# Kernel tuning notes

Measured on AMD Instinct MI355X. Metric: run time of the kernel, lower is better.

Reference implementation:

```python
import jax, jax.numpy as jnp
import numpy as np

KEHALF = 7.199822675975274  # half Coulomb constant, eV*Angstrom/e^2
SR_CUTOFF = 4.0
LR_CUTOFF = 10.0
N_ATOMS = 262144
N_PAIRS = 16777216


def setup_inputs() -> dict:
    key = jax.random.key(0)
    k1, k2, k3, k4 = jax.random.split(key, 4)
    # distances in (0.1, 12.1) Angstrom: spans both cutoffs, avoids r=0 singularity
    Dij = jax.random.uniform(k1, (N_PAIRS,), dtype=jnp.float32) * 12.0 + 0.1
    Qa = jax.random.normal(k2, (N_ATOMS,), dtype=jnp.float32) * 0.3  # partial charges
    idx_i = jax.random.randint(k3, (N_PAIRS,), 0, N_ATOMS, dtype=jnp.int64)
    idx_j = jax.random.randint(k4, (N_PAIRS,), 0, N_ATOMS, dtype=jnp.int64)
    return {"Dij": Dij, "Qa": Qa, "idx_i": idx_i, "idx_j": idx_j}


def _poly_cutoff(r, cutoff):
    x = r / cutoff
    return jnp.where(x < 1.0, 1.0 - x * x * x * (x * (6.0 * x - 15.0) + 10.0), 0.0)


def reference(Dij, Qa, idx_i, idx_j):
    lr2 = LR_CUTOFF * LR_CUTOFF
    Qi = Qa[idx_i]                      # [P]
    Qj = Qa[idx_j]                      # [P]
    Dij_sh = jnp.sqrt(Dij * Dij + 1.0)  # shielded distance
    switch = _poly_cutoff(Dij, SR_CUTOFF / 2.0)  # phi(2r) with cutoff sr
    cswitch = 1.0 - switch
    E_ord = 1.0 / Dij + Dij / lr2 - 2.0 / LR_CUTOFF
    E_sh = 1.0 / Dij_sh + Dij_sh / lr2 - 2.0 / LR_CUTOFF
    Eele = KEHALF * Qi * Qj * (switch * E_sh + cswitch * E_ord)
    Eele = jnp.where(Dij <= LR_CUTOFF, Eele, 0.0)
    # scatter-add per-pair energies to atoms
    return jax.ops.segment_sum(Eele, idx_i, num_segments=Qa.shape[0])
```

## Files before the change

kernel.cpp:

```cpp
#include <hip/hip_runtime.h>


#define KEHALF 7.199822675975274f
#define NB    128
#define BSH   11
#define BMASK 2047
#define CAP   126976
#define CURSTRIDE 16
#define SCH   2
#define SCAP  72
#define SSTR  73
#define VSCALE 524288.0f
#define VINV   (1.0f / 524288.0f)
#define P1B   512
#define P1PAIRS 8192

__device__ __forceinline__ float radial_fast(float d) {
    float d2p1 = d * d + 1.0f;
    float rsq  = __builtin_amdgcn_rsqf(d2p1);
    float x    = 0.5f * d;
    float sw   = (x < 1.0f) ? 1.0f - x * x * x * (x * (6.0f * x - 15.0f) + 10.0f)
                            : 0.0f;
    float Eo = __builtin_amdgcn_rcpf(d) + d * 0.01f - 0.2f;
    float Es = rsq * (1.0f + 0.01f * d2p1) - 0.2f;
    return sw * Es + (1.0f - sw) * Eo;
}

__global__ __launch_bounds__(P1B, 4) void ee_bin(
    const float* __restrict__ Dij,
    const float* __restrict__ Qa,
    const int*   __restrict__ idx_i,
    const int*   __restrict__ idx_j,
    unsigned int* __restrict__ list,
    unsigned int* __restrict__ gcur,
    float*        __restrict__ out)
{
    __shared__ unsigned int stage[NB * SSTR];
    __shared__ int lcur[NB + 32];
    __shared__ int gofs[NB];
    int tid = threadIdx.x;
    if (tid < NB + 32) lcur[tid] = 0;
    __syncthreads();

    long blockBase = (long)blockIdx.x * P1PAIRS;

    unsigned int EN[16];
    int          BK[16];
    int trash = NB + (tid & 31);
#pragma unroll
    for (int g = 0; g < 4; ++g) {
        long o = blockBase + ((long)(g * P1B + tid)) * 4;
        int4 j4 = *reinterpret_cast<const int4*>(idx_j + o);
        float qj0 = Qa[j4.x], qj1 = Qa[j4.y], qj2 = Qa[j4.z], qj3 = Qa[j4.w];
        float4 d4 = *reinterpret_cast<const float4*>(Dij + o);
        int4   i4 = *reinterpret_cast<const int4*>(idx_i + o);
        float dd[4] = {d4.x, d4.y, d4.z, d4.w};
        float qq[4] = {qj0, qj1, qj2, qj3};
        int   ii[4] = {i4.x, i4.y, i4.z, i4.w};
#pragma unroll
        for (int k = 0; k < 4; ++k) {
            int m = g * 4 + k;
            float d = dd[k];
            float w = qq[k] * radial_fast(d);
            int v = __float2int_rn(w * VSCALE);
            EN[m] = ((unsigned int)(ii[k] & BMASK) << 21) |
                    ((unsigned int)v & 0x1FFFFFu);
            BK[m] = (d <= 10.0f) ? (ii[k] >> BSH) : trash;
        }
    }

    int SL[16];
#pragma unroll
    for (int m = 0; m < 16; ++m)
        SL[m] = atomicAdd(&lcur[BK[m]], 1);

#pragma unroll
    for (int m = 0; m < 16; ++m) {
        if (BK[m] < NB) {
            if (SL[m] < SCAP) {
                stage[BK[m] * SSTR + SL[m]] = EN[m];
            } else {
                int atom = (BK[m] << BSH) | (int)(EN[m] >> 21);
                int v    = ((int)(EN[m] << 11)) >> 11;
                atomicAdd(out + atom, KEHALF * Qa[atom] * ((float)v * VINV));
            }
        }
    }
    __syncthreads();

    if (tid < NB) {
        int n = lcur[tid];
        if (n > SCAP) n = SCAP;
        lcur[tid] = n;
        int padded = (n + 3) & ~3;
        gofs[tid] = (int)atomicAdd(&gcur[tid * CURSTRIDE], (unsigned int)padded);
    }
    __syncthreads();

    int wave = tid >> 6, lane = tid & 63;
    for (int b = wave; b < NB; b += (P1B / 64)) {
        int n = lcur[b];
        int padded = (n + 3) & ~3;
        int go = gofs[b];
        long rb = (long)b * CAP;
        for (int i = lane; i < padded; i += 64) {
            unsigned int val = (i < n) ? stage[b * SSTR + i]
                                       : ((unsigned int)(i & BMASK) << 21);
            int pos = go + i;
            if (pos < CAP)
                list[rb + pos] = val;
        }
    }
}

__global__ __launch_bounds__(512) void ee_acc(
    const unsigned int* __restrict__ list,
    const unsigned int* __restrict__ gcur,
    int* __restrict__ partials)
{
    __shared__ int acc[1 << BSH];
    int b = blockIdx.x / SCH;
    int s = blockIdx.x % SCH;
    int t = threadIdx.x;
#pragma unroll
    for (int r = 0; r < (1 << BSH) / 512; ++r) acc[t + r * 512] = 0;
    __syncthreads();

    int n = (int)gcur[b * CURSTRIDE];
    if (n > CAP) n = CAP;
    int nq = n >> 2;
    int per = (nq + SCH - 1) / SCH;
    int q0 = s * per;
    int q1 = q0 + per; if (q1 > nq) q1 = nq;

    const uint4* lp4 = reinterpret_cast<const uint4*>(list + (long)b * CAP);
    for (int q = q0 + t; q < q1; q += 512) {
        uint4 u4 = lp4[q];
        unsigned int us[4] = {u4.x, u4.y, u4.z, u4.w};
#pragma unroll
        for (int k = 0; k < 4; ++k) {
            unsigned int u = us[k];
            int li = (int)(u >> 21);
            int v  = ((int)(u << 11)) >> 11;
            atomicAdd(&acc[li], v);
        }
    }
    __syncthreads();

    int* pp = partials + ((long)b * SCH + s) * (1 << BSH);
#pragma unroll
    for (int r = 0; r < (1 << BSH) / 512; ++r) pp[t + r * 512] = acc[t + r * 512];
}

__global__ __launch_bounds__(256) void ee_final(
    const int* __restrict__ partials,
    const float* __restrict__ Qa,
    float* __restrict__ out, int nAtoms)
{
    int q = blockIdx.x * blockDim.x + threadIdx.x;
    int n4 = nAtoms >> 2;
    if (q >= n4) return;
    int a0 = q << 2;
    int b  = a0 >> BSH;
    int li = a0 & BMASK;
    long base = (long)(b * SCH) * (1 << BSH) + li;
    int4 s = {0, 0, 0, 0};
#pragma unroll
    for (int r = 0; r < SCH; ++r) {
        int4 p = *reinterpret_cast<const int4*>(partials + base + (long)r * (1 << BSH));
        s.x += p.x; s.y += p.y; s.z += p.z; s.w += p.w;
    }
    float4 qv = reinterpret_cast<const float4*>(Qa)[q];
    float4 sp = reinterpret_cast<const float4*>(out)[q];
    float4 o;
    o.x = KEHALF * qv.x * ((float)s.x * VINV) + sp.x;
    o.y = KEHALF * qv.y * ((float)s.y * VINV) + sp.y;
    o.z = KEHALF * qv.z * ((float)s.z * VINV) + sp.z;
    o.w = KEHALF * qv.w * ((float)s.w * VINV) + sp.w;
    reinterpret_cast<float4*>(out)[q] = o;
}

#define FP_SCALE 4194304.0f
#define FP_INV   (1.0f / 4194304.0f)

__device__ __forceinline__ float radial_exact(float d) {
    float dsh = sqrtf(d * d + 1.0f);
    float x   = 0.5f * d;
    float sw  = (x < 1.0f) ? 1.0f - x * x * x * (x * (6.0f * x - 15.0f) + 10.0f)
                           : 0.0f;
    float Eo = 1.0f / d   + d   * 0.01f - 0.2f;
    float Es = 1.0f / dsh + dsh * 0.01f - 0.2f;
    return sw * Es + (1.0f - sw) * Eo;
}

__global__ __launch_bounds__(256) void ee_pair_fix(
    const float* __restrict__ Dij,
    const float* __restrict__ Qa,
    const int*   __restrict__ idx_i,
    const int*   __restrict__ idx_j,
    int*         __restrict__ acc,
    int P)
{
    long base = ((long)blockIdx.x * blockDim.x + threadIdx.x) * 4;
    if (base >= P) return;
    float4 d4 = *reinterpret_cast<const float4*>(Dij + base);
    int4   i4 = *reinterpret_cast<const int4*>(idx_i + base);
    int4   j4 = *reinterpret_cast<const int4*>(idx_j + base);
    float D[4]  = {d4.x, d4.y, d4.z, d4.w};
    int   ii[4] = {i4.x, i4.y, i4.z, i4.w};
    int   jj[4] = {j4.x, j4.y, j4.z, j4.w};
#pragma unroll
    for (int k = 0; k < 4; ++k) {
        float d = D[k];
        if (d > 10.0f) continue;
        float e = KEHALF * Qa[ii[k]] * Qa[jj[k]] * radial_exact(d);
        atomicAdd(acc + ii[k], __float2int_rn(e * FP_SCALE));
    }
}

__global__ __launch_bounds__(256) void ee_convert(
    const int* __restrict__ acc, float* __restrict__ out, int nAtoms)
{
    int n4 = nAtoms >> 2;
    int q = blockIdx.x * blockDim.x + threadIdx.x;
    if (q >= n4) return;
    int4 a = reinterpret_cast<const int4*>(acc)[q];
    float4 o;
    o.x = (float)a.x * FP_INV;
    o.y = (float)a.y * FP_INV;
    o.z = (float)a.z * FP_INV;
    o.w = (float)a.w * FP_INV;
    reinterpret_cast<float4*>(out)[q] = o;
}

__global__ __launch_bounds__(256) void ee_pair_direct(
    const float* __restrict__ Dij,
    const float* __restrict__ Qa,
    const int*   __restrict__ idx_i,
    const int*   __restrict__ idx_j,
    float*       __restrict__ out,
    int P)
{
    long t = (long)blockIdx.x * blockDim.x + threadIdx.x;
    if (t >= P) return;
    float d = Dij[t];
    if (d > 10.0f) return;
    atomicAdd(out + idx_i[t], KEHALF * Qa[idx_i[t]] * Qa[idx_j[t]] * radial_exact(d));
}

extern "C" void kernel_launch(void* const* d_in, const int* in_sizes, int n_in,
                              void* d_out, int out_size, void* d_ws, size_t ws_size,
                              hipStream_t stream) {
    const float* Dij   = (const float*)d_in[0];
    const float* Qa    = (const float*)d_in[1];
    const int*   idx_i = (const int*)d_in[2];
    const int*   idx_j = (const int*)d_in[3];
    float*       out   = (float*)d_out;

    int P      = in_sizes[0];
    int nAtoms = in_sizes[1];

    size_t listBytes = (size_t)NB * CAP * sizeof(unsigned int);
    size_t partBytes = (size_t)NB * SCH * (1 << BSH) * sizeof(int);
    size_t curBytes  = (size_t)NB * CURSTRIDE * sizeof(unsigned int);

    if (ws_size >= listBytes + partBytes + curBytes &&
        nAtoms == NB * (1 << BSH) && (P % P1PAIRS) == 0) {
        unsigned int* list = (unsigned int*)d_ws;
        int*          part = (int*)((char*)d_ws + listBytes);
        unsigned int* gcur = (unsigned int*)((char*)d_ws + listBytes + partBytes);
        hipMemsetAsync(gcur, 0, curBytes, stream);
        hipMemsetAsync(out, 0, (size_t)out_size * sizeof(float), stream);
        int grid1 = P / P1PAIRS;
        ee_bin<<<grid1, P1B, 0, stream>>>(Dij, Qa, idx_i, idx_j, list, gcur, out);
        ee_acc<<<NB * SCH, 512, 0, stream>>>(list, gcur, part);
        ee_final<<<(nAtoms / 4 + 255) / 256, 256, 0, stream>>>(part, Qa, out, nAtoms);
    } else if (ws_size >= (size_t)nAtoms * sizeof(int) &&
               (nAtoms & 3) == 0 && (P & 3) == 0) {
        int* acc = (int*)d_ws;
        hipMemsetAsync(acc, 0, (size_t)nAtoms * sizeof(int), stream);
        int grid = (P / 4 + 255) / 256;
        ee_pair_fix<<<grid, 256, 0, stream>>>(Dij, Qa, idx_i, idx_j, acc, P);
        ee_convert<<<(nAtoms / 4 + 255) / 256, 256, 0, stream>>>(acc, out, nAtoms);
    } else {
        hipMemsetAsync(out, 0, (size_t)out_size * sizeof(float), stream);
        int grid = (P + 255) / 256;
        ee_pair_direct<<<grid, 256, 0, stream>>>(Dij, Qa, idx_i, idx_j, out, P);
    }
}
```

Measured before the change: 272.8 us.

## Split radial weight computation into separate kernel with int16 weights

Adds a kernel that does the Qa[idx_j] gather and the radial function and writes a 16-bit quantized weight per pair, with a sentinel value for pairs beyond the cutoff. The binning kernel then reads only idx_i and the short weights. The aim is to separate the latency-bound random gather from the LDS-heavy binning so each kernel can reach its own occupancy. In exchange it adds an extra kernel launch and a 32 MB write and read-back of the weight array, and it coarsens quantization (scale 8192 shifted by 6, clamped at ±32000), which could cost accuracy.

```diff
diff --git a/kernel.cpp b/kernel.cpp
--- a/kernel.cpp
+++ b/kernel.cpp
@@ -12,8 +12,13 @@
 #define SSTR  73
 #define VSCALE 524288.0f
 #define VINV   (1.0f / 524288.0f)
+#define WSH   6
+#define WSCALE 8192.0f
+#define WSENT  (-32768)
 #define P1B   512
 #define P1PAIRS 8192
+#define RADB  256
+#define RADPAIRS 2048
 
 __device__ __forceinline__ float radial_fast(float d) {
     float d2p1 = d * d + 1.0f;
@@ -26,11 +31,39 @@
     return sw * Es + (1.0f - sw) * Eo;
 }
 
-__global__ __launch_bounds__(P1B, 4) void ee_bin(
+__global__ __launch_bounds__(RADB) void ee_radial(
     const float* __restrict__ Dij,
     const float* __restrict__ Qa,
+    const int*   __restrict__ idx_j,
+    short*       __restrict__ w)
+{
+    long blockBase = (long)blockIdx.x * RADPAIRS;
+    int tid = threadIdx.x;
+#pragma unroll
+    for (int g = 0; g < 2; ++g) {
+        long o = blockBase + (long)(g * RADB + tid) * 4;
+        int4   j4 = *reinterpret_cast<const int4*>(idx_j + o);
+        float qj0 = Qa[j4.x], qj1 = Qa[j4.y], qj2 = Qa[j4.z], qj3 = Qa[j4.w];
+        float4 d4 = *reinterpret_cast<const float4*>(Dij + o);
+        float dd[4] = {d4.x, d4.y, d4.z, d4.w};
+        float qq[4] = {qj0, qj1, qj2, qj3};
+        short s[4];
+#pragma unroll
+        for (int k = 0; k < 4; ++k) {
+            float wf = qq[k] * radial_fast(dd[k]) * WSCALE;
+            wf = fminf(fmaxf(wf, -32000.0f), 32000.0f);
+            int v = __float2int_rn(wf);
+            s[k] = (dd[k] <= 10.0f) ? (short)v : (short)WSENT;
+        }
+        short4 sv = {s[0], s[1], s[2], s[3]};
+        *reinterpret_cast<short4*>(w + o) = sv;
+    }
+}
+
+__global__ __launch_bounds__(P1B, 4) void ee_binw(
+    const short* __restrict__ w,
+    const float* __restrict__ Qa,
     const int*   __restrict__ idx_i,
-    const int*   __restrict__ idx_j,
     unsigned int* __restrict__ list,
     unsigned int* __restrict__ gcur,
     float*        __restrict__ out)
@@ -49,23 +82,18 @@
     int trash = NB + (tid & 31);
 #pragma unroll
     for (int g = 0; g < 4; ++g) {
-        long o = blockBase + ((long)(g * P1B + tid)) * 4;
-        int4 j4 = *reinterpret_cast<const int4*>(idx_j + o);
-        float qj0 = Qa[j4.x], qj1 = Qa[j4.y], qj2 = Qa[j4.z], qj3 = Qa[j4.w];
-        float4 d4 = *reinterpret_cast<const float4*>(Dij + o);
+        long o = blockBase + (long)(g * P1B + tid) * 4;
         int4   i4 = *reinterpret_cast<const int4*>(idx_i + o);
-        float dd[4] = {d4.x, d4.y, d4.z, d4.w};
-        float qq[4] = {qj0, qj1, qj2, qj3};
+        short4 w4 = *reinterpret_cast<const short4*>(w + o);
+        short ws[4] = {w4.x, w4.y, w4.z, w4.w};
         int   ii[4] = {i4.x, i4.y, i4.z, i4.w};
 #pragma unroll
         for (int k = 0; k < 4; ++k) {
             int m = g * 4 + k;
-            float d = dd[k];
-            float w = qq[k] * radial_fast(d);
-            int v = __float2int_rn(w * VSCALE);
+            int v = ((int)ws[k]) << WSH;
             EN[m] = ((unsigned int)(ii[k] & BMASK) << 21) |
                     ((unsigned int)v & 0x1FFFFFu);
-            BK[m] = (d <= 10.0f) ? (ii[k] >> BSH) : trash;
+            BK[m] = (ws[k] != WSENT) ? (ii[k] >> BSH) : trash;
         }
     }
 
@@ -113,6 +141,93 @@
     }
 }
 
+__global__ __launch_bounds__(P1B, 4) void ee_bin(
+    const float* __restrict__ Dij,
+    const float* __restrict__ Qa,
+    const int*   __restrict__ idx_i,
+    const int*   __restrict__ idx_j,
+    unsigned int* __restrict__ list,
+    unsigned int* __restrict__ gcur,
+    float*        __restrict__ out)
+{
+    __shared__ unsigned int stage[NB * SSTR];
+    __shared__ int lcur[NB + 32];
+    __shared__ int gofs[NB];
+    int tid = threadIdx.x;
+    if (tid < NB + 32) lcur[tid] = 0;
+    __syncthreads();
+
+    long blockBase = (long)blockIdx.x * P1PAIRS;
+
+    unsigned int EN[16];
+    int          BK[16];
+    int trash = NB + (tid & 31);
+#pragma unroll
+    for (int g = 0; g < 4; ++g) {
+        long o = blockBase + ((long)(g * P1B + tid)) * 4;
+        int4 j4 = *reinterpret_cast<const int4*>(idx_j + o);
+        float qj0 = Qa[j4.x], qj1 = Qa[j4.y], qj2 = Qa[j4.z], qj3 = Qa[j4.w];
+        float4 d4 = *reinterpret_cast<const float4*>(Dij + o);
+        int4   i4 = *reinterpret_cast<const int4*>(idx_i + o);
+        float dd[4] = {d4.x, d4.y, d4.z, d4.w};
+        float qq[4] = {qj0, qj1, qj2, qj3};
+        int   ii[4] = {i4.x, i4.y, i4.z, i4.w};
+#pragma unroll
+        for (int k = 0; k < 4; ++k) {
+            int m = g * 4 + k;
+            float d = dd[k];
+            float ww = qq[k] * radial_fast(d);
+            int v = __float2int_rn(ww * VSCALE);
+            EN[m] = ((unsigned int)(ii[k] & BMASK) << 21) |
+                    ((unsigned int)v & 0x1FFFFFu);
+            BK[m] = (d <= 10.0f) ? (ii[k] >> BSH) : trash;
+        }
+    }
+
+    int SL[16];
+#pragma unroll
+    for (int m = 0; m < 16; ++m)
+        SL[m] = atomicAdd(&lcur[BK[m]], 1);
+
+#pragma unroll
+    for (int m = 0; m < 16; ++m) {
+        if (BK[m] < NB) {
+            if (SL[m] < SCAP) {
+                stage[BK[m] * SSTR + SL[m]] = EN[m];
+            } else {
+                int atom = (BK[m] << BSH) | (int)(EN[m] >> 21);
+                int v    = ((int)(EN[m] << 11)) >> 11;
+                atomicAdd(out + atom, KEHALF * Qa[atom] * ((float)v * VINV));
+            }
+        }
+    }
+    __syncthreads();
+
+    if (tid < NB) {
+        int n = lcur[tid];
+        if (n > SCAP) n = SCAP;
+        lcur[tid] = n;
+        int padded = (n + 3) & ~3;
+        gofs[tid] = (int)atomicAdd(&gcur[tid * CURSTRIDE], (unsigned int)padded);
+    }
+    __syncthreads();
+
+    int wave = tid >> 6, lane = tid & 63;
+    for (int b = wave; b < NB; b += (P1B / 64)) {
+        int n = lcur[b];
+        int padded = (n + 3) & ~3;
+        int go = gofs[b];
+        long rb = (long)b * CAP;
+        for (int i = lane; i < padded; i += 64) {
+            unsigned int val = (i < n) ? stage[b * SSTR + i]
+                                       : ((unsigned int)(i & BMASK) << 21);
+            int pos = go + i;
+            if (pos < CAP)
+                list[rb + pos] = val;
+        }
+    }
+}
+
 __global__ __launch_bounds__(512) void ee_acc(
     const unsigned int* __restrict__ list,
     const unsigned int* __restrict__ gcur,
@@ -263,16 +378,30 @@
     size_t listBytes = (size_t)NB * CAP * sizeof(unsigned int);
     size_t partBytes = (size_t)NB * SCH * (1 << BSH) * sizeof(int);
     size_t curBytes  = (size_t)NB * CURSTRIDE * sizeof(unsigned int);
-
-    if (ws_size >= listBytes + partBytes + curBytes &&
-        nAtoms == NB * (1 << BSH) && (P % P1PAIRS) == 0) {
+    size_t wBytes    = (size_t)P * sizeof(short);
+    size_t baseBytes = listBytes + partBytes + curBytes;
+
+    if (ws_size >= baseBytes + wBytes &&
+        nAtoms == NB * (1 << BSH) && (P % P1PAIRS) == 0 &&
+        (P % RADPAIRS) == 0) {
+        unsigned int* list = (unsigned int*)d_ws;
+        int*          part = (int*)((char*)d_ws + listBytes);
+        unsigned int* gcur = (unsigned int*)((char*)d_ws + listBytes + partBytes);
+        short*        wbuf = (short*)((char*)d_ws + baseBytes);
+        hipMemsetAsync(gcur, 0, curBytes, stream);
+        hipMemsetAsync(out, 0, (size_t)out_size * sizeof(float), stream);
+        ee_radial<<<P / RADPAIRS, RADB, 0, stream>>>(Dij, Qa, idx_j, wbuf);
+        ee_binw<<<P / P1PAIRS, P1B, 0, stream>>>(wbuf, Qa, idx_i, list, gcur, out);
+        ee_acc<<<NB * SCH, 512, 0, stream>>>(list, gcur, part);
+        ee_final<<<(nAtoms / 4 + 255) / 256, 256, 0, stream>>>(part, Qa, out, nAtoms);
+    } else if (ws_size >= baseBytes &&
+               nAtoms == NB * (1 << BSH) && (P % P1PAIRS) == 0) {
         unsigned int* list = (unsigned int*)d_ws;
         int*          part = (int*)((char*)d_ws + listBytes);
         unsigned int* gcur = (unsigned int*)((char*)d_ws + listBytes + partBytes);
         hipMemsetAsync(gcur, 0, curBytes, stream);
         hipMemsetAsync(out, 0, (size_t)out_size * sizeof(float), stream);
-        int grid1 = P / P1PAIRS;
-        ee_bin<<<grid1, P1B, 0, stream>>>(Dij, Qa, idx_i, idx_j, list, gcur, out);
+        ee_bin<<<P / P1PAIRS, P1B, 0, stream>>>(Dij, Qa, idx_i, idx_j, list, gcur, out);
         ee_acc<<<NB * SCH, 512, 0, stream>>>(list, gcur, part);
         ee_final<<<(nAtoms / 4 + 255) / 256, 256, 0, stream>>>(part, Qa, out, nAtoms);
     } else if (ws_size >= (size_t)nAtoms * sizeof(int) &&
```

Result: slower. 312.6 us (+14.6%).
